# Optimization experiments

Hardware: AMD Instinct MI355X
Metric: run time of the kernel (lower is better)

## Reference

```python
import jax, jax.numpy as jnp
import numpy as np

D, A, B, R, N, E, NENT, L = 128, 64, 8, 200, 100000, 800000, 50000, 2
SLOPE = (0.125 + 1.0 / 3.0) / 2.0  # RReLU eval-mode slope (lower+upper)/2
EPS = 1e-5


def _ln(x, g, b):
    mu = jnp.mean(x, axis=-1, keepdims=True)
    v = jnp.mean((x - mu) ** 2, axis=-1, keepdims=True)
    return (x - mu) * jax.lax.rsqrt(v + EPS) * g + b


def _rrelu(x):
    return jnp.where(x >= 0, x, SLOPE * x)


def setup_inputs() -> dict:
    key = jax.random.key(0)
    ks = jax.random.split(key, 32)
    s = 0.05
    inp = {
        'hidden': jax.random.normal(ks[0], (N, D), jnp.float32),
        'rel_emb': jax.random.normal(ks[1], (B * (R + 1), D), jnp.float32),
        'batch_idx': jax.random.randint(ks[2], (E,), 0, B, jnp.int32),
        'rel': jax.random.randint(ks[3], (E,), 0, R + 1, jnp.int32),
        'sub': jax.random.randint(ks[4], (E,), 0, N, jnp.int32),
        'obj': jax.random.randint(ks[5], (E,), 0, N, jnp.int32),
        'q_rel': jax.random.randint(ks[6], (B,), 0, R + 1, jnp.int32),
        'nodes_batch': jax.random.randint(ks[7], (N,), 0, B, jnp.int32),
        'nodes_ent': jax.random.randint(ks[8], (N,), 0, NENT, jnp.int32),
        # per-layer params (stacked over L); stored as [in, out]
        'Ws': jax.random.normal(ks[9], (L, D, A)) * s,
        'Wr': jax.random.normal(ks[10], (L, D, A)) * s,
        'Wqr_w': jax.random.normal(ks[11], (L, D, A)) * s,
        'Wqr_b': jnp.zeros((L, A)),
        'Walpha_w': jax.random.normal(ks[12], (L, A)) * s,
        'Walpha_b': jnp.zeros((L,)),
        'Wh': jax.random.normal(ks[13], (L, D, D)) * s,
        'rt_w': jax.random.normal(ks[14], (L, D, D)) * s,
        'rt_b': jnp.zeros((L, D)),
        'ln_g': jnp.ones((L, D)), 'ln_b': jnp.zeros((L, D)),
        'lnr_g': jnp.ones((L, D)), 'lnr_b': jnp.zeros((L, D)),
        # shared GRU (PyTorch layout: [3D, D], gates r,z,n)
        'gru_wih': jax.random.normal(ks[15], (3 * D, D)) * s,
        'gru_whh': jax.random.normal(ks[16], (3 * D, D)) * s,
        'gru_bih': jnp.zeros((3 * D,)),
        'gru_bhh': jnp.zeros((3 * D,)),
        'Wfinal': jax.random.normal(ks[17], (D,)) * s,
    }
    return inp


def _gru_step(x, h, wih, whh, bih, bhh):
    gi = x @ wih.T + bih
    gh = h @ whh.T + bhh
    i_r, i_z, i_n = jnp.split(gi, 3, axis=-1)
    h_r, h_z, h_n = jnp.split(gh, 3, axis=-1)
    r = jax.nn.sigmoid(i_r + h_r)
    z = jax.nn.sigmoid(i_z + h_z)
    n = jnp.tanh(i_n + r * h_n)
    return (1.0 - z) * n + z * h


def reference(hidden, rel_emb, Ws, Wr, Wqr_w, Wqr_b, Walpha_w, Walpha_b, Wh,
              rt_w, rt_b, ln_g, ln_b, lnr_g, lnr_b,
              gru_wih, gru_whh, gru_bih, gru_bhh, Wfinal,
              batch_idx, rel, sub, obj, q_rel, nodes_batch, nodes_ent):
    h0 = jnp.zeros_like(hidden)
    rel_flat_idx = rel + batch_idx * (R + 1)  # [E]
    q_flat_idx = q_rel + jnp.arange(B, dtype=q_rel.dtype) * (R + 1)  # [B]
    for i in range(L):
        # relation transfer + residual + LN
        re_ = jax.nn.relu(rel_emb @ rt_w[i] + rt_b[i])
        rel_emb = _ln(rel_emb + re_, lnr_g[i], lnr_b[i])
        # GNN layer: edge-wise gather
        hs = hidden[sub]                       # [E, D]
        hr = rel_emb[rel_flat_idx]             # [E, D]
        h_qr = rel_emb[q_flat_idx][batch_idx]  # [E, D]
        pre = hs @ Ws[i] + hr @ Wr[i] + h_qr @ Wqr_w[i] + Wqr_b[i]  # [E, A]
        alpha = jax.nn.sigmoid(_rrelu(pre) @ Walpha_w[i] + Walpha_b[i])  # [E]
        msg = alpha[:, None] * (hs + hr)       # [E, D]
        agg = jax.ops.segment_sum(msg, obj, num_segments=N)  # [N, D]
        hidden = _rrelu(agg @ Wh[i])
        hidden = _ln(hidden, ln_g[i], ln_b[i])
        hidden = _gru_step(hidden, h0, gru_wih, gru_whh, gru_bih, gru_bhh)
        h0 = hidden
        rel_emb = _ln(rel_emb, lnr_g[i], lnr_b[i])
    scores = hidden @ Wfinal  # [N]
    scores_all = jnp.zeros((B, NENT), dtype=scores.dtype).at[nodes_batch, nodes_ent].set(scores)
    return scores_all
```

## Files before the change

### kernel.cpp

```cpp
#include <hip/hip_runtime.h>
#include <hip/hip_bf16.h>

constexpr int DD = 128;
constexpr int AA = 64;
constexpr int GG = 384;
constexpr int XPAD = 136;
constexpr int GTS = 192;

#define SLOPE_F 0.22916666666666666f
#define LNEPS   1e-5f

typedef __attribute__((ext_vector_type(8))) short short8;
typedef __attribute__((ext_vector_type(4))) float f32x4;

static __device__ __forceinline__ float wave_sum(float v){
#pragma unroll
  for (int off = 32; off > 0; off >>= 1) v += __shfl_xor(v, off, 64);
  return v;
}
static __device__ __forceinline__ float red16(float v){
#pragma unroll
  for (int off = 1; off < 16; off <<= 1) v += __shfl_xor(v, off, 64);
  return v;
}
static __device__ __forceinline__ float sigm(float x){ return 1.0f / (1.0f + __expf(-x)); }
static __device__ __forceinline__ float rrelu_f(float x){ return x >= 0.0f ? x : SLOPE_F * x; }
static __device__ __forceinline__ short bf16b(float f){
  __hip_bfloat16 h = __float2bfloat16(f);
  return *reinterpret_cast<short*>(&h);
}
static __device__ __forceinline__ float b2f_lo(unsigned int x){
  return __uint_as_float(x << 16);
}
static __device__ __forceinline__ float b2f_hi(unsigned int x){
  return __uint_as_float(x & 0xffff0000u);
}
static __device__ __forceinline__ short8 ld_frag_f32(const float* p){
  float4 f0 = *(const float4*)p;
  float4 f1 = *(const float4*)(p + 4);
  short8 v;
  v[0]=bf16b(f0.x); v[1]=bf16b(f0.y); v[2]=bf16b(f0.z); v[3]=bf16b(f0.w);
  v[4]=bf16b(f1.x); v[5]=bf16b(f1.y); v[6]=bf16b(f1.z); v[7]=bf16b(f1.w);
  return v;
}

template<bool PRE_LN>
__global__ void __launch_bounds__(256) k_rel_transfer(float* __restrict__ rel,
    const float* __restrict__ rtw, const float* __restrict__ rtb,
    const float* __restrict__ g, const float* __restrict__ b,
    const float* __restrict__ gp, const float* __restrict__ bp, int rows){
  __shared__ float xrow[4][DD];
  float* xl = xrow[threadIdx.x >> 6];
  const int lane = threadIdx.x & 63;
  int wave = (int)((blockIdx.x * blockDim.x + threadIdx.x) >> 6);
  if (wave >= rows) return;
  int row = __builtin_amdgcn_readfirstlane(wave);
  float* x = rel + (size_t)row * DD;
  float t0 = x[lane], t1 = x[64 + lane];
  if (PRE_LN){
    float mu = wave_sum(t0 + t1) * (1.0f/128.0f);
    float e0 = t0 - mu, e1 = t1 - mu;
    float var = wave_sum(e0*e0 + e1*e1) * (1.0f/128.0f);
    float rs = rsqrtf(var + LNEPS);
    t0 = e0 * rs * gp[lane]      + bp[lane];
    t1 = e1 * rs * gp[64 + lane] + bp[64 + lane];
  }
  xl[lane] = t0; xl[64 + lane] = t1;
  float y0 = 0.f, y1 = 0.f;
#pragma unroll 4
  for (int d = 0; d < DD; ++d){
    float xd = xl[d];
    y0 = fmaf(xd, rtw[d*DD + lane],      y0);
    y1 = fmaf(xd, rtw[d*DD + 64 + lane], y1);
  }
  float u0 = t0 + fmaxf(y0 + rtb[lane],      0.f);
  float u1 = t1 + fmaxf(y1 + rtb[64 + lane], 0.f);
  float mu = wave_sum(u0 + u1) * (1.0f/128.0f);
  float e0 = u0 - mu, e1 = u1 - mu;
  float var = wave_sum(e0*e0 + e1*e1) * (1.0f/128.0f);
  float rs = rsqrtf(var + LNEPS);
  x[lane]      = e0 * rs * g[lane]      + b[lane];
  x[64 + lane] = e1 * rs * g[64 + lane] + b[64 + lane];
}

__global__ void __launch_bounds__(256) k_prep_bfrag_km(const float* __restrict__ W,
    short* __restrict__ out, int C, int ldc){
  int idx = blockIdx.x * blockDim.x + threadIdx.x;
  int total = (C >> 4) * 4 * 64;
  if (idx >= total) return;
  int lane = idx & 63, ks = (idx >> 6) & 3, ct = idx >> 8;
  int k = ks*32 + ((lane >> 4) << 3);
  int c = (ct << 4) + (lane & 15);
  short8 v;
#pragma unroll
  for (int j = 0; j < 8; ++j) v[j] = bf16b(W[(size_t)(k + j)*ldc + c]);
  *reinterpret_cast<short8*>(out + (size_t)idx * 8) = v;
}

__global__ void __launch_bounds__(256) k_prep_bfrag(const float* __restrict__ W,
    short* __restrict__ out, int Nc){
  int idx = blockIdx.x * blockDim.x + threadIdx.x;
  int total = (Nc >> 4) * 4 * 64;
  if (idx >= total) return;
  int lane = idx & 63, ks = (idx >> 6) & 3, ct = idx >> 8;
  int k = ks*32 + ((lane >> 4) << 3);
  int c = (ct << 4) + (lane & 15);
  const float* src = W + (size_t)c * DD + k;
  short8 v;
#pragma unroll
  for (int j = 0; j < 8; ++j) v[j] = bf16b(src[j]);
  *reinterpret_cast<short8*>(out + (size_t)idx * 8) = v;
}

__global__ void __launch_bounds__(256) k_proj_gt(const float* __restrict__ X,
    const short* __restrict__ Bf, unsigned short* __restrict__ GT, int rows){
  const int lane = threadIdx.x & 63;
  int wave = (int)((blockIdx.x * blockDim.x + threadIdx.x) >> 6);
  int r0 = wave * 16;
  if (r0 >= rows) return;
  if (r0 + 16 > rows) r0 = rows - 16;
  r0 = __builtin_amdgcn_readfirstlane(r0);
  const int arow = lane & 15;
  const int koff = (lane >> 4) << 3;
  short8 ax[4];
#pragma unroll
  for (int ks = 0; ks < 4; ++ks){
    ax[ks] = ld_frag_f32(X + (size_t)(r0 + arow) * DD + ks*32 + koff);
    *reinterpret_cast<short8*>((short*)GT + (size_t)(r0 + arow) * GTS + 64 + ks*32 + koff) = ax[ks];
  }
  f32x4 acc[4];
#pragma unroll
  for (int ct = 0; ct < 4; ++ct){
    acc[ct] = (f32x4)0.f;
#pragma unroll
    for (int ks = 0; ks < 4; ++ks){
      short8 bw = *reinterpret_cast<const short8*>(Bf + ((size_t)(ct*4 + ks)*64 + lane)*8);
      acc[ct] = __builtin_amdgcn_mfma_f32_16x16x32_bf16(ax[ks], bw, acc[ct], 0, 0, 0);
    }
  }
#pragma unroll
  for (int ct = 0; ct < 4; ++ct){
    int col = ct*16 + (lane & 15);
#pragma unroll
    for (int reg = 0; reg < 4; ++reg){
      int row = r0 + ((lane >> 4) << 2) + reg;
      ((short*)GT)[(size_t)row*GTS + col] = bf16b(acc[ct][reg]);
    }
  }
}

__global__ void __launch_bounds__(256) k_projq(const float* __restrict__ rel,
    const float* __restrict__ Wqr, const float* __restrict__ bias,
    const int* __restrict__ q_rel, float* __restrict__ out, int Bc, int Rp1){
  const int lane = threadIdx.x & 63;
  int wave = (int)((blockIdx.x * blockDim.x + threadIdx.x) >> 6);
  if (wave >= Bc) return;
  int b = __builtin_amdgcn_readfirstlane(wave);
  int f = __builtin_amdgcn_readfirstlane(q_rel[b] + b * Rp1);
  const float* x = rel + (size_t)f * DD;
  float a = 0.f;
#pragma unroll 4
  for (int d = 0; d < DD; ++d) a = fmaf(x[d], Wqr[d*AA + lane], a);
  out[(size_t)b*AA + lane] = a + bias[lane];
}

__global__ void __launch_bounds__(256) k_hist(const int* __restrict__ obj, int* __restrict__ deg, int E){
  int idx = blockIdx.x * blockDim.x + threadIdx.x;
  if (idx < E) atomicAdd(&deg[obj[idx]], 1);
}

__global__ void __launch_bounds__(1024) k_scan1(const int* __restrict__ deg,
    int* __restrict__ row_start, int* __restrict__ bsum, int n){
  __shared__ int sm[1024];
  int t = threadIdx.x;
  int i = blockIdx.x * 1024 + t;
  int v = (i < n) ? deg[i] : 0;
  sm[t] = v; __syncthreads();
#pragma unroll
  for (int off = 1; off < 1024; off <<= 1){
    int x = (t >= off) ? sm[t - off] : 0;
    __syncthreads();
    sm[t] += x;
    __syncthreads();
  }
  if (i < n) row_start[i] = sm[t] - v;
  if (t == 1023) bsum[blockIdx.x] = sm[1023];
}

__global__ void __launch_bounds__(1024) k_scan2(int* __restrict__ bsum, int nb){
  __shared__ int sm[1024];
  int t = threadIdx.x;
  int v = (t < nb) ? bsum[t] : 0;
  sm[t] = v; __syncthreads();
#pragma unroll
  for (int off = 1; off < 1024; off <<= 1){
    int x = (t >= off) ? sm[t - off] : 0;
    __syncthreads();
    sm[t] += x;
    __syncthreads();
  }
  if (t < nb) bsum[t] = sm[t] - v;
}

__global__ void __launch_bounds__(256) k_scan3(int* __restrict__ row_start,
    const int* __restrict__ bsum, int n, int E){
  int i = blockIdx.x * blockDim.x + threadIdx.x;
  if (i < n) row_start[i] += bsum[i >> 10];
  if (i == 0) row_start[n] = E;
}

__global__ void __launch_bounds__(256) k_scatter_edges(const int* __restrict__ obj,
    const int* __restrict__ sub, const int* __restrict__ bidx,
    const int* __restrict__ reli, const int* __restrict__ row_start,
    int* __restrict__ cursor, unsigned int* __restrict__ ER, int E, int Rp1){
  int e = blockIdx.x * blockDim.x + threadIdx.x;
  if (e < E){
    int o = obj[e];
    int pos = row_start[o] + atomicAdd(&cursor[o], 1);
    int bb = bidx[e];
    unsigned rec = (unsigned)sub[e] | ((unsigned)(reli[e] + bb * Rp1) << 17)
                 | ((unsigned)bb << 28);
    ER[pos] = rec;
  }
}

__global__ void __launch_bounds__(256) k_edge_csr4(
    const unsigned short* __restrict__ GT, const unsigned short* __restrict__ RT,
    const float* __restrict__ qr,
    const float* __restrict__ wal, const float* __restrict__ walb_p,
    const unsigned int* __restrict__ ER, const int* __restrict__ row_start,
    float* __restrict__ agg, int Nn){
  const int lane = threadIdx.x & 63;
  const int g = lane >> 4;
  const int t = lane & 15;
  int wave = (int)((blockIdx.x * blockDim.x + threadIdx.x) >> 6);
  if (wave >= Nn) return;
  int o = __builtin_amdgcn_readfirstlane(wave);
  const int s0 = __builtin_amdgcn_readfirstlane(row_start[o]);
  const int s1 = __builtin_amdgcn_readfirstlane(row_start[o + 1]);
  const float4 wa4 = *reinterpret_cast<const float4*>(wal + t*4);
  const float wb = walb_p[0];
  float acc[8];
#pragma unroll
  for (int i = 0; i < 8; ++i) acc[i] = 0.f;
  for (int base = s0; base < s1; base += 8){
    int pA = base + g;
    int pB = base + g + 4;
    bool vA = pA < s1, vB = pB < s1;
    unsigned eA = ER[vA ? pA : s0];
    unsigned eB = ER[vB ? pB : s0];
    int sA = eA & 0x1FFFF, fA = (eA >> 17) & 0x7FF, bA = eA >> 28;
    int sB = eB & 0x1FFFF, fB = (eB >> 17) & 0x7FF, bB = eB >> 28;
    const unsigned short* gsA = GT + (size_t)sA * GTS;
    const unsigned short* rfA = RT + (size_t)fA * GTS;
    const unsigned short* gsB = GT + (size_t)sB * GTS;
    const unsigned short* rfB = RT + (size_t)fB * GTS;
    uint2 pgA = *reinterpret_cast<const uint2*>(gsA + t*4);
    uint2 prA = *reinterpret_cast<const uint2*>(rfA + t*4);
    float4 q4A = *reinterpret_cast<const float4*>(qr + (size_t)bA*AA + t*4);
    uint4 xgA = *reinterpret_cast<const uint4*>(gsA + 64 + t*8);
    uint4 xrA = *reinterpret_cast<const uint4*>(rfA + 64 + t*8);
    uint2 pgB = *reinterpret_cast<const uint2*>(gsB + t*4);
    uint2 prB = *reinterpret_cast<const uint2*>(rfB + t*4);
    float4 q4B = *reinterpret_cast<const float4*>(qr + (size_t)bB*AA + t*4);
    uint4 xgB = *reinterpret_cast<const uint4*>(gsB + 64 + t*8);
    uint4 xrB = *reinterpret_cast<const uint4*>(rfB + 64 + t*8);
    float pA0 = b2f_lo(pgA.x) + b2f_lo(prA.x) + q4A.x;
    float pA1 = b2f_hi(pgA.x) + b2f_hi(prA.x) + q4A.y;
    float pA2 = b2f_lo(pgA.y) + b2f_lo(prA.y) + q4A.z;
    float pA3 = b2f_hi(pgA.y) + b2f_hi(prA.y) + q4A.w;
    float dotA = rrelu_f(pA0)*wa4.x + rrelu_f(pA1)*wa4.y
               + rrelu_f(pA2)*wa4.z + rrelu_f(pA3)*wa4.w;
    float pB0 = b2f_lo(pgB.x) + b2f_lo(prB.x) + q4B.x;
    float pB1 = b2f_hi(pgB.x) + b2f_hi(prB.x) + q4B.y;
    float pB2 = b2f_lo(pgB.y) + b2f_lo(prB.y) + q4B.z;
    float pB3 = b2f_hi(pgB.y) + b2f_hi(prB.y) + q4B.w;
    float dotB = rrelu_f(pB0)*wa4.x + rrelu_f(pB1)*wa4.y
               + rrelu_f(pB2)*wa4.z + rrelu_f(pB3)*wa4.w;
#pragma unroll
    for (int off = 1; off < 16; off <<= 1){
      dotA += __shfl_xor(dotA, off, 64);
      dotB += __shfl_xor(dotB, off, 64);
    }
    float alA = vA ? sigm(dotA + wb) : 0.f;
    float alB = vB ? sigm(dotB + wb) : 0.f;
    acc[0] = fmaf(alA, b2f_lo(xgA.x) + b2f_lo(xrA.x), fmaf(alB, b2f_lo(xgB.x) + b2f_lo(xrB.x), acc[0]));
    acc[1] = fmaf(alA, b2f_hi(xgA.x) + b2f_hi(xrA.x), fmaf(alB, b2f_hi(xgB.x) + b2f_hi(xrB.x), acc[1]));
    acc[2] = fmaf(alA, b2f_lo(xgA.y) + b2f_lo(xrA.y), fmaf(alB, b2f_lo(xgB.y) + b2f_lo(xrB.y), acc[2]));
    acc[3] = fmaf(alA, b2f_hi(xgA.y) + b2f_hi(xrA.y), fmaf(alB, b2f_hi(xgB.y) + b2f_hi(xrB.y), acc[3]));
    acc[4] = fmaf(alA, b2f_lo(xgA.z) + b2f_lo(xrA.z), fmaf(alB, b2f_lo(xgB.z) + b2f_lo(xrB.z), acc[4]));
    acc[5] = fmaf(alA, b2f_hi(xgA.z) + b2f_hi(xrA.z), fmaf(alB, b2f_hi(xgB.z) + b2f_hi(xrB.z), acc[5]));
    acc[6] = fmaf(alA, b2f_lo(xgA.w) + b2f_lo(xrA.w), fmaf(alB, b2f_lo(xgB.w) + b2f_lo(xrB.w), acc[6]));
    acc[7] = fmaf(alA, b2f_hi(xgA.w) + b2f_hi(xrA.w), fmaf(alB, b2f_hi(xgB.w) + b2f_hi(xrB.w), acc[7]));
  }
#pragma unroll
  for (int i = 0; i < 8; ++i){
    acc[i] += __shfl_xor(acc[i], 16, 64);
    acc[i] += __shfl_xor(acc[i], 32, 64);
  }
  if (g == 0){
    float4 v0 = make_float4(acc[0], acc[1], acc[2], acc[3]);
    float4 v1 = make_float4(acc[4], acc[5], acc[6], acc[7]);
    *reinterpret_cast<float4*>(agg + (size_t)o*DD + t*8)     = v0;
    *reinterpret_cast<float4*>(agg + (size_t)o*DD + t*8 + 4) = v1;
  }
}

template<bool HAS_H>
__global__ void __launch_bounds__(256) k_whlngru(const float* __restrict__ AGG,
    float* H, const short* __restrict__ Bwh, const short* __restrict__ Bih,
    const short* __restrict__ Bhh, const float* __restrict__ lng,
    const float* __restrict__ lnb, const float* __restrict__ bih,
    const float* __restrict__ bhh, int rows){
  __shared__ short xtile[4 * 16 * XPAD];
  short* xl = xtile + (threadIdx.x >> 6) * 16 * XPAD;
  const int lane = threadIdx.x & 63;
  int wave = (int)((blockIdx.x * blockDim.x + threadIdx.x) >> 6);
  if (wave * 16 >= rows) return;
  int r0 = wave * 16;
  if (r0 + 16 > rows) r0 = rows - 16;
  r0 = __builtin_amdgcn_readfirstlane(r0);
  const int arow = lane & 15;
  const int koff = (lane >> 4) << 3;
  const int lrbase = (lane >> 4) << 2;

  short8 aa[4];
#pragma unroll
  for (int ks = 0; ks < 4; ++ks)
    aa[ks] = ld_frag_f32(AGG + (size_t)(r0 + arow) * DD + ks*32 + koff);
  f32x4 acc[8];
#pragma unroll
  for (int ct = 0; ct < 8; ++ct){
    acc[ct] = (f32x4)0.f;
#pragma unroll
    for (int ks = 0; ks < 4; ++ks){
      short8 bw = *reinterpret_cast<const short8*>(Bwh + ((size_t)(ct*4 + ks)*64 + lane)*8);
      acc[ct] = __builtin_amdgcn_mfma_f32_16x16x32_bf16(aa[ks], bw, acc[ct], 0, 0, 0);
    }
  }
#pragma unroll
  for (int ct = 0; ct < 8; ++ct)
#pragma unroll
    for (int reg = 0; reg < 4; ++reg) acc[ct][reg] = rrelu_f(acc[ct][reg]);

  float mu[4], rs[4];
#pragma unroll
  for (int reg = 0; reg < 4; ++reg){
    float s = 0.f, ss = 0.f;
#pragma unroll
    for (int ct = 0; ct < 8; ++ct){ float v = acc[ct][reg]; s += v; ss += v*v; }
    s = red16(s); ss = red16(ss);
    float m = s * (1.0f/128.0f);
    float var = ss * (1.0f/128.0f) - m*m;
    mu[reg] = m;
    rs[reg] = rsqrtf(var + LNEPS);
  }
#pragma unroll
  for (int ct = 0; ct < 8; ++ct){
    int col = ct*16 + (lane & 15);
    float gv = lng[col], bv = lnb[col];
#pragma unroll
    for (int reg = 0; reg < 4; ++reg){
      float xn = (acc[ct][reg] - mu[reg]) * rs[reg] * gv + bv;
      xl[(lrbase + reg) * XPAD + col] = bf16b(xn);
    }
  }

  short8 ax[4], ah8[4];
#pragma unroll
  for (int ks = 0; ks < 4; ++ks)
    ax[ks] = *reinterpret_cast<const short8*>(&xl[arow * XPAD + ks*32 + koff]);
  if (HAS_H){
#pragma unroll
    for (int ks = 0; ks < 4; ++ks)
      ah8[ks] = ld_frag_f32(H + (size_t)(r0 + arow) * DD + ks*32 + koff);
  }

#pragma unroll
  for (int ct = 0; ct < 8; ++ct){
    f32x4 air = (f32x4)0.f, aiz = (f32x4)0.f, ain = (f32x4)0.f;
    f32x4 ahr = (f32x4)0.f, ahz = (f32x4)0.f, ahn = (f32x4)0.f;
#pragma unroll
    for (int ks = 0; ks < 4; ++ks){
      short8 b0 = *reinterpret_cast<const short8*>(Bih + ((size_t)((0*8 + ct)*4 + ks)*64 + lane)*8);
      short8 b1 = *reinterpret_cast<const short8*>(Bih + ((size_t)((8 + ct)*4 + ks)*64 + lane)*8);
      short8 b2 = *reinterpret_cast<const short8*>(Bih + ((size_t)((16 + ct)*4 + ks)*64 + lane)*8);
      air = __builtin_amdgcn_mfma_f32_16x16x32_bf16(ax[ks], b0, air, 0, 0, 0);
      aiz = __builtin_amdgcn_mfma_f32_16x16x32_bf16(ax[ks], b1, aiz, 0, 0, 0);
      ain = __builtin_amdgcn_mfma_f32_16x16x32_bf16(ax[ks], b2, ain, 0, 0, 0);
      if (HAS_H){
        short8 c0 = *reinterpret_cast<const short8*>(Bhh + ((size_t)((0*8 + ct)*4 + ks)*64 + lane)*8);
        short8 c1 = *reinterpret_cast<const short8*>(Bhh + ((size_t)((8 + ct)*4 + ks)*64 + lane)*8);
        short8 c2 = *reinterpret_cast<const short8*>(Bhh + ((size_t)((16 + ct)*4 + ks)*64 + lane)*8);
        ahr = __builtin_amdgcn_mfma_f32_16x16x32_bf16(ah8[ks], c0, ahr, 0, 0, 0);
        ahz = __builtin_amdgcn_mfma_f32_16x16x32_bf16(ah8[ks], c1, ahz, 0, 0, 0);
        ahn = __builtin_amdgcn_mfma_f32_16x16x32_bf16(ah8[ks], c2, ahn, 0, 0, 0);
      }
    }
    int col = ct*16 + (lane & 15);
    float bi_r = bih[col], bi_z = bih[128 + col], bi_n = bih[256 + col];
    float bh_r = bhh[col], bh_z = bhh[128 + col], bh_n = bhh[256 + col];
#pragma unroll
    for (int reg = 0; reg < 4; ++reg){
      int row = r0 + lrbase + reg;
      float gi_r = air[reg] + bi_r;
      float gi_z = aiz[reg] + bi_z;
      float gi_n = ain[reg] + bi_n;
      float gh_r = (HAS_H ? ahr[reg] : 0.f) + bh_r;
      float gh_z = (HAS_H ? ahz[reg] : 0.f) + bh_z;
      float gh_n = (HAS_H ? ahn[reg] : 0.f) + bh_n;
      float rg = sigm(gi_r + gh_r);
      float zg = sigm(gi_z + gh_z);
      float ng = tanhf(gi_n + rg * gh_n);
      float hp = HAS_H ? H[(size_t)row * DD + col] : 0.f;
      H[(size_t)row * DD + col] = (1.f - zg) * ng + zg * hp;
    }
  }
}

__global__ void __launch_bounds__(256) k_score(const float* __restrict__ Hf,
    const float* __restrict__ wf, const int* __restrict__ nb, const int* __restrict__ ne,
    float* __restrict__ scores, int* __restrict__ winner, int rows, int NENT){
  const int lane = threadIdx.x & 63;
  int wave = (int)((blockIdx.x * blockDim.x + threadIdx.x) >> 6);
  if (wave >= rows) return;
  int row = __builtin_amdgcn_readfirstlane(wave);
  float v = Hf[(size_t)row*DD + lane] * wf[lane] + Hf[(size_t)row*DD + 64 + lane] * wf[64 + lane];
  float s = wave_sum(v);
  if (lane == 0){
    scores[row] = s;
    int slot = nb[row] * NENT + ne[row];
    atomicMax(&winner[slot], row);
  }
}

__global__ void __launch_bounds__(256) k_scatter(const float* __restrict__ scores,
    const int* __restrict__ winner, const int* __restrict__ nb, const int* __restrict__ ne,
    float* __restrict__ out, int rows, int NENT){
  int n = blockIdx.x * blockDim.x + threadIdx.x;
  if (n < rows){
    int slot = nb[n] * NENT + ne[n];
    if (winner[slot] == n) out[slot] = scores[n];
  }
}

extern "C" void kernel_launch(void* const* d_in, const int* in_sizes, int n_in,
                              void* d_out, int out_size, void* d_ws, size_t ws_size,
                              hipStream_t stream){
  const float* hidden0 = (const float*)d_in[0];
  const float* rel0    = (const float*)d_in[1];
  const int* batch_idx = (const int*)d_in[2];
  const int* rel_i     = (const int*)d_in[3];
  const int* sub       = (const int*)d_in[4];
  const int* obj       = (const int*)d_in[5];
  const int* q_rel     = (const int*)d_in[6];
  const int* nb        = (const int*)d_in[7];
  const int* ne        = (const int*)d_in[8];
  const float* Ws      = (const float*)d_in[9];
  const float* Wr      = (const float*)d_in[10];
  const float* Wqr_w   = (const float*)d_in[11];
  const float* Wqr_b   = (const float*)d_in[12];
  const float* Wal_w   = (const float*)d_in[13];
  const float* Wal_b   = (const float*)d_in[14];
  const float* Wh      = (const float*)d_in[15];
  const float* rt_w    = (const float*)d_in[16];
  const float* rt_b    = (const float*)d_in[17];
  const float* ln_g    = (const float*)d_in[18];
  const float* ln_b    = (const float*)d_in[19];
  const float* lnr_g   = (const float*)d_in[20];
  const float* lnr_b   = (const float*)d_in[21];
  const float* wih     = (const float*)d_in[22];
  const float* whh     = (const float*)d_in[23];
  const float* bih     = (const float*)d_in[24];
  const float* bhh     = (const float*)d_in[25];
  const float* wfin    = (const float*)d_in[26];

  const int N    = in_sizes[0] / DD;
  const int NR   = in_sizes[1] / DD;
  const int E    = in_sizes[2];
  const int Bc   = in_sizes[6];
  const int L    = in_sizes[14];
  const int Rp1  = NR / Bc;
  const int NENT = out_size / Bc;

  char* wsp = (char*)d_ws;
  auto alloc = [&](size_t bytes) -> void* {
    void* p = (void*)wsp;
    wsp += (bytes + 255) & ~(size_t)255;
    return p;
  };
  float* AGG     = (float*)alloc((size_t)N * DD * 4);
  float* HBUF    = (float*)alloc((size_t)N * DD * 4);
  float* rel_cur = (float*)alloc((size_t)NR * DD * 4);
  unsigned short* GT = (unsigned short*)alloc((size_t)N * GTS * 2);
  unsigned short* RT = (unsigned short*)alloc((size_t)NR * GTS * 2);
  float* qr      = (float*)alloc((size_t)Bc * AA * 4);
  short* Bih     = (short*)alloc((size_t)(GG/16) * 4 * 64 * 8 * 2);
  short* Bhh     = (short*)alloc((size_t)(GG/16) * 4 * 64 * 8 * 2);
  short* Bws     = (short*)alloc((size_t)L * 4 * 4 * 64 * 8 * 2);
  short* Bwr     = (short*)alloc((size_t)L * 4 * 4 * 64 * 8 * 2);
  short* Bwh     = (short*)alloc((size_t)L * 8 * 4 * 64 * 8 * 2);
  float* scores  = (float*)alloc((size_t)N * 4);
  int*   winner  = (int*)alloc((size_t)Bc * NENT * 4);
  int*   deg     = (int*)alloc((size_t)N * 4);
  int*   row_st  = (int*)alloc((size_t)(N + 1) * 4);
  int*   cursor  = (int*)alloc((size_t)N * 4);
  unsigned int* ER = (unsigned int*)alloc((size_t)E * 4);
  int*   bsum    = (int*)alloc((size_t)1024 * 4);
  (void)ws_size; (void)n_in;

  hipMemcpyAsync(rel_cur, rel0, (size_t)NR * DD * 4, hipMemcpyDeviceToDevice, stream);
  {
    int totg = (GG/16) * 4 * 64;
    k_prep_bfrag<<<(totg + 255)/256, 256, 0, stream>>>(wih, Bih, GG);
    k_prep_bfrag<<<(totg + 255)/256, 256, 0, stream>>>(whh, Bhh, GG);
    int tot64 = 4 * 4 * 64;
    int tot128 = 8 * 4 * 64;
    for (int i = 0; i < L; ++i){
      k_prep_bfrag_km<<<(tot64 + 255)/256, 256, 0, stream>>>(Ws + (size_t)i*DD*AA, Bws + (size_t)i*tot64*8, AA, AA);
      k_prep_bfrag_km<<<(tot64 + 255)/256, 256, 0, stream>>>(Wr + (size_t)i*DD*AA, Bwr + (size_t)i*tot64*8, AA, AA);
      k_prep_bfrag_km<<<(tot128 + 255)/256, 256, 0, stream>>>(Wh + (size_t)i*DD*DD, Bwh + (size_t)i*tot128*8, DD, DD);
    }
  }
  hipMemsetAsync(d_out, 0, (size_t)out_size * 4, stream);
  hipMemsetAsync(winner, 0xFF, (size_t)Bc * NENT * 4, stream);

  hipMemsetAsync(deg, 0, (size_t)N * 4, stream);
  hipMemsetAsync(cursor, 0, (size_t)N * 4, stream);
  k_hist<<<(E + 255)/256, 256, 0, stream>>>(obj, deg, E);
  {
    int nb1 = (N + 1023)/1024;
    k_scan1<<<nb1, 1024, 0, stream>>>(deg, row_st, bsum, N);
    k_scan2<<<1, 1024, 0, stream>>>(bsum, nb1);
    k_scan3<<<(N + 255)/256, 256, 0, stream>>>(row_st, bsum, N, E);
  }
  k_scatter_edges<<<(E + 255)/256, 256, 0, stream>>>(obj, sub, batch_idx, rel_i,
      row_st, cursor, ER, E, Rp1);

  const float* hid_in = hidden0;
  auto blocks4 = [](int waves){ return (waves + 3) / 4; };
  const int tot64 = 4 * 4 * 64;
  const int tot128 = 8 * 4 * 64;

  for (int i = 0; i < L; ++i){
    if (i == 0)
      k_rel_transfer<false><<<blocks4(NR), 256, 0, stream>>>(rel_cur,
          rt_w + (size_t)i*DD*DD, rt_b + (size_t)i*DD,
          lnr_g + (size_t)i*DD, lnr_b + (size_t)i*DD,
          nullptr, nullptr, NR);
    else
      k_rel_transfer<true><<<blocks4(NR), 256, 0, stream>>>(rel_cur,
          rt_w + (size_t)i*DD*DD, rt_b + (size_t)i*DD,
          lnr_g + (size_t)i*DD, lnr_b + (size_t)i*DD,
          lnr_g + (size_t)(i-1)*DD, lnr_b + (size_t)(i-1)*DD, NR);
    k_proj_gt<<<blocks4((N+15)/16), 256, 0, stream>>>(hid_in, Bws + (size_t)i*tot64*8, GT, N);
    k_proj_gt<<<blocks4((NR+15)/16), 256, 0, stream>>>(rel_cur, Bwr + (size_t)i*tot64*8, RT, NR);
    k_projq<<<blocks4(Bc), 256, 0, stream>>>(rel_cur, Wqr_w + (size_t)i*DD*AA,
        Wqr_b + (size_t)i*AA, q_rel, qr, Bc, Rp1);
    k_edge_csr4<<<blocks4(N), 256, 0, stream>>>(GT, RT, qr,
        Wal_w + (size_t)i*AA, Wal_b + i, ER, row_st, AGG, N);
    {
      int waves = (N + 15)/16;
      if (i == 0)
        k_whlngru<false><<<blocks4(waves), 256, 0, stream>>>(AGG, HBUF,
            Bwh + (size_t)i*tot128*8, Bih, Bhh,
            ln_g + (size_t)i*DD, ln_b + (size_t)i*DD, bih, bhh, N);
      else
        k_whlngru<true><<<blocks4(waves), 256, 0, stream>>>(AGG, HBUF,
            Bwh + (size_t)i*tot128*8, Bih, Bhh,
            ln_g + (size_t)i*DD, ln_b + (size_t)i*DD, bih, bhh, N);
    }
    hid_in = HBUF;
  }

  k_score<<<blocks4(N), 256, 0, stream>>>(hid_in, wfin, nb, ne, scores, winner, N, NENT);
  k_scatter<<<(N + 255)/256, 256, 0, stream>>>(scores, winner, nb, ne, (float*)d_out, N, NENT);
}
```

Baseline: 498.5 us.

## Stage GRU weight fragments in double-buffered LDS shared across block waves

The GRU part of the fused Wh/LN/GRU kernel now loads each column tile of the input and hidden weight fragments into a double-buffered shared-memory buffer. The four waves in a block split the copy, so each wave no longer fetches every B fragment from global memory on its own. Dead waves are kept alive so they can take part in the block barriers. tanhf is also replaced with an exp-based fast tanh. The cost is one __syncthreads per tile step, extra LDS use that may lower occupancy, and slightly different tanh precision.

```diff
diff --git a/kernel.cpp b/kernel.cpp
--- a/kernel.cpp
+++ b/kernel.cpp
@@ -24,6 +24,12 @@
   return v;
 }
 static __device__ __forceinline__ float sigm(float x){ return 1.0f / (1.0f + __expf(-x)); }
+static __device__ __forceinline__ float fast_tanh(float x){
+  float ax = fabsf(x);
+  float t = __expf(-2.0f * ax);
+  float r = (1.0f - t) / (1.0f + t);
+  return copysignf(r, x);
+}
 static __device__ __forceinline__ float rrelu_f(float x){ return x >= 0.0f ? x : SLOPE_F * x; }
 static __device__ __forceinline__ short bf16b(float f){
   __hip_bfloat16 h = __float2bfloat16(f);
@@ -313,16 +319,33 @@
     const float* __restrict__ lnb, const float* __restrict__ bih,
     const float* __restrict__ bhh, int rows){
   __shared__ short xtile[4 * 16 * XPAD];
+  __shared__ short wbuf[2][12 * 512];
   short* xl = xtile + (threadIdx.x >> 6) * 16 * XPAD;
   const int lane = threadIdx.x & 63;
+  const int wib  = threadIdx.x >> 6;
   int wave = (int)((blockIdx.x * blockDim.x + threadIdx.x) >> 6);
-  if (wave * 16 >= rows) return;
-  int r0 = wave * 16;
+  const bool live = (wave * 16 < rows);
+  int r0 = live ? wave * 16 : 0;
   if (r0 + 16 > rows) r0 = rows - 16;
   r0 = __builtin_amdgcn_readfirstlane(r0);
   const int arow = lane & 15;
   const int koff = (lane >> 4) << 3;
   const int lrbase = (lane >> 4) << 2;
+  constexpr int NU = HAS_H ? 16 : 8;
+
+  auto stage = [&](int u, int par){
+    int ct = HAS_H ? (u >> 1) : u;
+    const short* src = (HAS_H && (u & 1)) ? Bhh : Bih;
+#pragma unroll
+    for (int jj = 0; jj < 3; ++jj){
+      int j = wib * 3 + jj;
+      int gfrag = (j >> 2) * 32 + ct * 4 + (j & 3);
+      *reinterpret_cast<short8*>(&wbuf[par][j * 512 + lane * 8]) =
+          *reinterpret_cast<const short8*>(src + (size_t)gfrag * 512 + lane * 8);
+    }
+  };
+
+  stage(0, 0);
 
   short8 aa[4];
 #pragma unroll
@@ -376,45 +399,56 @@
       ah8[ks] = ld_frag_f32(H + (size_t)(r0 + arow) * DD + ks*32 + koff);
   }
 
-#pragma unroll
-  for (int ct = 0; ct < 8; ++ct){
-    f32x4 air = (f32x4)0.f, aiz = (f32x4)0.f, ain = (f32x4)0.f;
-    f32x4 ahr = (f32x4)0.f, ahz = (f32x4)0.f, ahn = (f32x4)0.f;
+  __syncthreads();
+
+  f32x4 air = (f32x4)0.f, aiz = (f32x4)0.f, ain = (f32x4)0.f;
+  f32x4 ahr = (f32x4)0.f, ahz = (f32x4)0.f, ahn = (f32x4)0.f;
+#pragma unroll
+  for (int u = 0; u < NU; ++u){
+    if (u + 1 < NU) stage(u + 1, (u + 1) & 1);
+    const short* wb = wbuf[u & 1];
+    const bool is_hh = HAS_H && (u & 1);
+    const int ct = HAS_H ? (u >> 1) : u;
+    if (!is_hh){
+      air = (f32x4)0.f; aiz = (f32x4)0.f; ain = (f32x4)0.f;
+      ahr = (f32x4)0.f; ahz = (f32x4)0.f; ahn = (f32x4)0.f;
+    }
 #pragma unroll
     for (int ks = 0; ks < 4; ++ks){
-      short8 b0 = *reinterpret_cast<const short8*>(Bih + ((size_t)((0*8 + ct)*4 + ks)*64 + lane)*8);
-      short8 b1 = *reinterpret_cast<const short8*>(Bih + ((size_t)((8 + ct)*4 + ks)*64 + lane)*8);
-      short8 b2 = *reinterpret_cast<const short8*>(Bih + ((size_t)((16 + ct)*4 + ks)*64 + lane)*8);
-      air = __builtin_amdgcn_mfma_f32_16x16x32_bf16(ax[ks], b0, air, 0, 0, 0);
-      aiz = __builtin_amdgcn_mfma_f32_16x16x32_bf16(ax[ks], b1, aiz, 0, 0, 0);
-      ain = __builtin_amdgcn_mfma_f32_16x16x32_bf16(ax[ks], b2, ain, 0, 0, 0);
-      if (HAS_H){
-        short8 c0 = *reinterpret_cast<const short8*>(Bhh + ((size_t)((0*8 + ct)*4 + ks)*64 + lane)*8);
-        short8 c1 = *reinterpret_cast<const short8*>(Bhh + ((size_t)((8 + ct)*4 + ks)*64 + lane)*8);
-        short8 c2 = *reinterpret_cast<const short8*>(Bhh + ((size_t)((16 + ct)*4 + ks)*64 + lane)*8);
-        ahr = __builtin_amdgcn_mfma_f32_16x16x32_bf16(ah8[ks], c0, ahr, 0, 0, 0);
-        ahz = __builtin_amdgcn_mfma_f32_16x16x32_bf16(ah8[ks], c1, ahz, 0, 0, 0);
-        ahn = __builtin_amdgcn_mfma_f32_16x16x32_bf16(ah8[ks], c2, ahn, 0, 0, 0);
+      short8 b0 = *reinterpret_cast<const short8*>(&wb[(0*4 + ks)*512 + lane*8]);
+      short8 b1 = *reinterpret_cast<const short8*>(&wb[(1*4 + ks)*512 + lane*8]);
+      short8 b2 = *reinterpret_cast<const short8*>(&wb[(2*4 + ks)*512 + lane*8]);
+      if (!is_hh){
+        air = __builtin_amdgcn_mfma_f32_16x16x32_bf16(ax[ks], b0, air, 0, 0, 0);
+        aiz = __builtin_amdgcn_mfma_f32_16x16x32_bf16(ax[ks], b1, aiz, 0, 0, 0);
+        ain = __builtin_amdgcn_mfma_f32_16x16x32_bf16(ax[ks], b2, ain, 0, 0, 0);
+      } else {
+        ahr = __builtin_amdgcn_mfma_f32_16x16x32_bf16(ah8[ks], b0, ahr, 0, 0, 0);
+        ahz = __builtin_amdgcn_mfma_f32_16x16x32_bf16(ah8[ks], b1, ahz, 0, 0, 0);
+        ahn = __builtin_amdgcn_mfma_f32_16x16x32_bf16(ah8[ks], b2, ahn, 0, 0, 0);
       }
     }
-    int col = ct*16 + (lane & 15);
-    float bi_r = bih[col], bi_z = bih[128 + col], bi_n = bih[256 + col];
-    float bh_r = bhh[col], bh_z = bhh[128 + col], bh_n = bhh[256 + col];
-#pragma unroll
-    for (int reg = 0; reg < 4; ++reg){
-      int row = r0 + lrbase + reg;
-      float gi_r = air[reg] + bi_r;
-      float gi_z = aiz[reg] + bi_z;
-      float gi_n = ain[reg] + bi_n;
-      float gh_r = (HAS_H ? ahr[reg] : 0.f) + bh_r;
-      float gh_z = (HAS_H ? ahz[reg] : 0.f) + bh_z;
-      float gh_n = (HAS_H ? ahn[reg] : 0.f) + bh_n;
-      float rg = sigm(gi_r + gh_r);
-      float zg = sigm(gi_z + gh_z);
-      float ng = tanhf(gi_n + rg * gh_n);
-      float hp = HAS_H ? H[(size_t)row * DD + col] : 0.f;
-      H[(size_t)row * DD + col] = (1.f - zg) * ng + zg * hp;
-    }
+    if (!HAS_H || is_hh){
+      int col = ct*16 + (lane & 15);
+      float bi_r = bih[col], bi_z = bih[128 + col], bi_n = bih[256 + col];
+      float bh_r = bhh[col], bh_z = bhh[128 + col], bh_n = bhh[256 + col];
+#pragma unroll
+      for (int reg = 0; reg < 4; ++reg){
+        int row = r0 + lrbase + reg;
+        float gi_r = air[reg] + bi_r;
+        float gi_z = aiz[reg] + bi_z;
+        float gi_n = ain[reg] + bi_n;
+        float gh_r = (HAS_H ? ahr[reg] : 0.f) + bh_r;
+        float gh_z = (HAS_H ? ahz[reg] : 0.f) + bh_z;
+        float gh_n = (HAS_H ? ahn[reg] : 0.f) + bh_n;
+        float rg = sigm(gi_r + gh_r);
+        float zg = sigm(gi_z + gh_z);
+        float ng = fast_tanh(gi_n + rg * gh_n);
+        float hp = HAS_H ? H[(size_t)row * DD + col] : 0.f;
+        if (live) H[(size_t)row * DD + col] = (1.f - zg) * ng + zg * hp;
+      }
+    }
+    __syncthreads();
   }
 }
 
```

After: 473.4 us. 1.05x faster.
